# Kernel optimization log

Measured on AMD Instinct MI355X. Metric: run time of the kernel, lower is better.

The kernel has to match this reference:

```python
import jax, jax.numpy as jnp
import numpy as np

SEQ_LEN, IN_DIM = 120, 132
UNITS = (64, 128, 64)
N_LABELS = 101


def _lstm(x, W, U, b):
    """Keras-style LSTM with activation='relu', recurrent_activation='sigmoid'.
    x: (B,T,D), W: (D,4u), U: (u,4u), b: (4u,). Gate order i,f,c,o.
    Returns full hidden sequence (B,T,u)."""
    u = U.shape[0]
    # precompute input projections for all timesteps (big GEMM outside scan)
    xz = jnp.einsum('btd,dz->btz', x, W) + b  # (B,T,4u)

    def step(carry, z_t):
        h, c = carry
        z = z_t + h @ U  # (B,4u)
        i, f, g, o = jnp.split(z, 4, axis=-1)
        i = jax.nn.sigmoid(i)
        f = jax.nn.sigmoid(f)
        o = jax.nn.sigmoid(o)
        c = f * c + i * jax.nn.relu(g)
        h = o * jax.nn.relu(c)
        return (h, c), h

    B = x.shape[0]
    h0 = jnp.zeros((B, u), x.dtype)
    (_, _), hs = jax.lax.scan(step, (h0, h0), jnp.swapaxes(xz, 0, 1))
    return jnp.swapaxes(hs, 0, 1)  # (B,T,u)


def setup_inputs() -> dict:
    key = jax.random.key(0)
    ks = jax.random.split(key, 16)
    s = 0.05
    d = {'x': jax.random.normal(ks[0], (1024, SEQ_LEN, IN_DIM), jnp.float32)}
    in_dims = (IN_DIM,) + UNITS[:-1]
    for l, (din, u) in enumerate(zip(in_dims, UNITS), start=1):
        d[f'W{l}'] = jax.random.normal(ks[3 * l - 2], (din, 4 * u), jnp.float32) * s
        d[f'U{l}'] = jax.random.normal(ks[3 * l - 1], (u, 4 * u), jnp.float32) * s
        d[f'b{l}'] = jnp.zeros((4 * u,), jnp.float32)
    dense_dims = [(UNITS[-1], 64), (64, 32), (32, N_LABELS)]
    for l, (din, dout) in enumerate(dense_dims, start=1):
        d[f'Wd{l}'] = jax.random.normal(ks[9 + l], (din, dout), jnp.float32) * s
        d[f'bd{l}'] = jnp.zeros((dout,), jnp.float32)
    return d


def reference(x, W1, U1, b1, W2, U2, b2, W3, U3, b3,
              Wd1, bd1, Wd2, bd2, Wd3, bd3):
    h = _lstm(x, W1, U1, b1)          # (B,T,64)
    h = _lstm(h, W2, U2, b2)          # (B,T,128)
    h = _lstm(h, W3, U3, b3)[:, -1]   # return_sequences=False -> (B,64)
    h = jax.nn.relu(h @ Wd1 + bd1)    # (B,64)
    h = jax.nn.relu(h @ Wd2 + bd2)    # (B,32)
    return jax.nn.softmax(h @ Wd3 + bd3, axis=-1)  # (B,101)
```

## Files before the change

### kernel.cpp

```cpp
#include <hip/hip_runtime.h>
#include <math.h>

#define T_STEPS 120
#define BATCH   1024

typedef __attribute__((ext_vector_type(8))) short bf16x8;
typedef __attribute__((ext_vector_type(4))) float f32x4;
typedef unsigned short u16;

__device__ __forceinline__ unsigned split2(float f) {
    union { float f; unsigned u; } a; a.f = f;
    unsigned hi = a.u >> 16;
    union { float f; unsigned u; } h; h.u = a.u & 0xFFFF0000u;
    union { float f; unsigned u; } b; b.f = f - h.f;
    unsigned rr = b.u + 0x7FFFu + ((b.u >> 16) & 1);
    return (hi << 16) | (rr >> 16);
}

__device__ __forceinline__ short bf16rne(float f) {
    union { float f; unsigned u; } a; a.f = f;
    unsigned r = a.u + 0x7FFFu + ((a.u >> 16) & 1);
    return (short)(r >> 16);
}

__device__ __forceinline__ float fast_sigmoid(float x) {
    float e = __expf(-x);
    return __builtin_amdgcn_rcpf(1.f + e);
}

__device__ __forceinline__ void block_sync_lds() {
    asm volatile("s_waitcnt lgkmcnt(0)" ::: "memory");
    __builtin_amdgcn_sched_barrier(0);
    __builtin_amdgcn_s_barrier();
    __builtin_amdgcn_sched_barrier(0);
}

__global__ __launch_bounds__(256)
void xconv(const float* __restrict__ x, u16* __restrict__ xhi)
{
    int idx = blockIdx.x * 256 + threadIdx.x;
    int k   = idx % 144;
    int bt  = idx / 144;
    float f = (k < 132) ? x[(size_t)bt * 132 + k] : 0.f;
    xhi[idx] = (u16)(unsigned short)bf16rne(f);
}

template<int U, int KXD, int KTX, int KTAIL, int TPB, bool XLO, bool LAST_ONLY>
__global__ __launch_bounds__(TPB, 1)
void lstm_fused(const u16* __restrict__ xhi, const u16* __restrict__ xlo,
                const float* __restrict__ W, int KIN,
                const float* __restrict__ Uw, const float* __restrict__ bias,
                u16* __restrict__ hhi, u16* __restrict__ hlo,
                float* __restrict__ hlast)
{
    constexpr int NZ  = 4 * U;
    constexpr int KTH = U / 32;
    constexpr int NB  = 16;
    constexpr int HPLANE = NB * U;
    constexpr int NGRP = U / 16;
    constexpr int XPSTRIDE = 20;
    static_assert(TPB == NGRP * 128, "h-waves + x-waves");

    __shared__ u16 hsh[4 * HPLANE];
    __shared__ float xp[2 * NZ * XPSTRIDE];

    const int tid  = threadIdx.x;
    const int lane = tid & 63;
    const int wid  = tid >> 6;
    const int ln   = lane & 15;
    const int lq   = lane >> 4;
    const bool ish = (wid < NGRP);
    const int g    = ish ? wid : wid - NGRP;
    const int unit = g * 16 + ln;
    const int b0   = blockIdx.x * NB;

    if (ish) {
        bf16x8 bwu[4][KTH];
#pragma unroll
        for (int p = 0; p < 4; ++p)
#pragma unroll
            for (int kt = 0; kt < KTH; ++kt)
#pragma unroll
                for (int e = 0; e < 8; ++e) {
                    int k = kt * 32 + lq * 8 + e;
                    bwu[p][kt][e] = bf16rne(Uw[(size_t)k * NZ + p * U + unit]);
                }
        float breg[4];
#pragma unroll
        for (int p = 0; p < 4; ++p) breg[p] = bias[p * U + unit];

        u16* hw0 = hsh + ((unit >> 3) * NB + lq * 4) * 8 + (unit & 7);
        u16* hw1 = hw0 + 2 * HPLANE;
        float creg[4];
#pragma unroll
        for (int r = 0; r < 4; ++r) {
            creg[r] = 0.f;
            hw0[r * 8] = 0;
            hw0[HPLANE + r * 8] = 0;
        }

        const u16* hrd[2][KTH];
#pragma unroll
        for (int b = 0; b < 2; ++b)
#pragma unroll
            for (int kt = 0; kt < KTH; ++kt)
                hrd[b][kt] = hsh + b * 2 * HPLANE + ((kt * 4 + lq) * NB + ln) * 8;

        const float* xprd[2];
        xprd[0] = xp;
        xprd[1] = xp + (size_t)NZ * XPSTRIDE;

        size_t ho = ((size_t)(b0 + lq * 4) * T_STEPS) * U + unit;

        block_sync_lds();

#define HSTEP(CUR, OTH, tc)                                                     \
    {                                                                           \
        f32x4 acc[4];                                                           \
        _Pragma("unroll")                                                       \
        for (int p = 0; p < 4; ++p) {                                           \
            f32x4 v = *reinterpret_cast<const f32x4*>(                          \
                xprd[CUR] + (p * U + unit) * XPSTRIDE + lq * 4);                \
            acc[p][0] = v[0] + breg[p]; acc[p][1] = v[1] + breg[p];             \
            acc[p][2] = v[2] + breg[p]; acc[p][3] = v[3] + breg[p];             \
        }                                                                       \
        _Pragma("unroll")                                                       \
        for (int kt = 0; kt < KTH; ++kt) {                                      \
            bf16x8 ahh = *reinterpret_cast<const bf16x8*>(hrd[CUR][kt]);        \
            bf16x8 ahl = *reinterpret_cast<const bf16x8*>(hrd[CUR][kt] + HPLANE); \
            _Pragma("unroll")                                                   \
            for (int p = 0; p < 4; ++p) {                                       \
                acc[p] = __builtin_amdgcn_mfma_f32_16x16x32_bf16(ahh, bwu[p][kt], acc[p], 0, 0, 0); \
                acc[p] = __builtin_amdgcn_mfma_f32_16x16x32_bf16(ahl, bwu[p][kt], acc[p], 0, 0, 0); \
            }                                                                   \
        }                                                                       \
        _Pragma("unroll")                                                       \
        for (int r = 0; r < 4; ++r) {                                           \
            float si = fast_sigmoid(acc[0][r]);                                 \
            float sf = fast_sigmoid(acc[1][r]);                                 \
            float gg = fmaxf(acc[2][r], 0.f);                                   \
            float so = fast_sigmoid(acc[3][r]);                                 \
            float c  = sf * creg[r] + si * gg;                                  \
            creg[r] = c;                                                        \
            float h = so * fmaxf(c, 0.f);                                       \
            unsigned s = split2(h);                                             \
            u16* hw = (OTH) ? hw1 : hw0;                                        \
            hw[r * 8] = (u16)(s >> 16);                                         \
            hw[HPLANE + r * 8] = (u16)s;                                        \
            if constexpr (!LAST_ONLY) {                                         \
                size_t o = ho + (size_t)r * (T_STEPS * U) + (size_t)(tc) * U;   \
                hhi[o] = (u16)(s >> 16);                                        \
                hlo[o] = (u16)s;                                                \
            } else {                                                            \
                if ((tc) == T_STEPS - 1)                                        \
                    hlast[(size_t)(b0 + lq * 4 + r) * U + unit] = h;            \
            }                                                                   \
        }                                                                       \
        block_sync_lds();                                                       \
    }

        for (int t = 0; t < T_STEPS; t += 2) {
            HSTEP(0, 1, t)
            HSTEP(1, 0, t + 1)
        }
#undef HSTEP
    } else {
        bf16x8 wxw[KTX][4];
#pragma unroll
        for (int kt = 0; kt < KTX; ++kt)
#pragma unroll
            for (int p = 0; p < 4; ++p)
#pragma unroll
                for (int e = 0; e < 8; ++e) {
                    int k = kt * 32 + lq * 8 + e;
                    wxw[kt][p][e] = (k < KIN) ? bf16rne(W[(size_t)k * NZ + p * U + unit])
                                              : (short)0;
                }

        const u16* pxh = xhi + ((size_t)(b0 + ln) * T_STEPS) * KXD + lq * 8;
        const u16* pxl = XLO ? (xlo + ((size_t)(b0 + ln) * T_STEPS) * KXD + lq * 8) : nullptr;

        float* xpw[2];
        xpw[0] = xp;
        xpw[1] = xp + (size_t)NZ * XPSTRIDE;

        bf16x8 xfh[KTX] = {}, xfl[KTX] = {};
#pragma unroll
        for (int kt = 0; kt < KTX; ++kt)
            if (kt < KTX - 1 || lq < KTAIL) {
                xfh[kt] = *reinterpret_cast<const bf16x8*>(pxh + kt * 32);
                if constexpr (XLO)
                    xfl[kt] = *reinterpret_cast<const bf16x8*>(pxl + kt * 32);
            }

        {
            f32x4 xacc[4] = {};
#pragma unroll
            for (int kt = 0; kt < KTX; ++kt)
#pragma unroll
                for (int p = 0; p < 4; ++p) {
                    xacc[p] = __builtin_amdgcn_mfma_f32_16x16x32_bf16(xfh[kt], wxw[kt][p], xacc[p], 0, 0, 0);
                    if constexpr (XLO)
                        xacc[p] = __builtin_amdgcn_mfma_f32_16x16x32_bf16(xfl[kt], wxw[kt][p], xacc[p], 0, 0, 0);
                }
#pragma unroll
            for (int p = 0; p < 4; ++p)
                *reinterpret_cast<f32x4*>(xpw[0] + (p * U + unit) * XPSTRIDE + lq * 4) = xacc[p];
            pxh += KXD; if constexpr (XLO) pxl += KXD;
#pragma unroll
            for (int kt = 0; kt < KTX; ++kt)
                if (kt < KTX - 1 || lq < KTAIL) {
                    xfh[kt] = *reinterpret_cast<const bf16x8*>(pxh + kt * 32);
                    if constexpr (XLO)
                        xfl[kt] = *reinterpret_cast<const bf16x8*>(pxl + kt * 32);
                }
        }

        block_sync_lds();

#define XSTEP(OTH, tc)                                                          \
    {                                                                           \
        if ((tc) + 1 < T_STEPS) {                                               \
            f32x4 xacc[4] = {};                                                 \
            _Pragma("unroll")                                                   \
            for (int kt = 0; kt < KTX; ++kt)                                    \
            _Pragma("unroll")                                                   \
            for (int p = 0; p < 4; ++p) {                                       \
                xacc[p] = __builtin_amdgcn_mfma_f32_16x16x32_bf16(xfh[kt], wxw[kt][p], xacc[p], 0, 0, 0); \
                if constexpr (XLO)                                              \
                    xacc[p] = __builtin_amdgcn_mfma_f32_16x16x32_bf16(xfl[kt], wxw[kt][p], xacc[p], 0, 0, 0); \
            }                                                                   \
            _Pragma("unroll")                                                   \
            for (int p = 0; p < 4; ++p)                                         \
                *reinterpret_cast<f32x4*>(xpw[OTH] + (p * U + unit) * XPSTRIDE + lq * 4) = xacc[p]; \
            if ((tc) + 2 < T_STEPS) {                                           \
                pxh += KXD; if constexpr (XLO) pxl += KXD;                      \
                _Pragma("unroll")                                               \
                for (int kt = 0; kt < KTX; ++kt)                                \
                    if (kt < KTX - 1 || lq < KTAIL) {                           \
                        xfh[kt] = *reinterpret_cast<const bf16x8*>(pxh + kt * 32); \
                        if constexpr (XLO)                                      \
                            xfl[kt] = *reinterpret_cast<const bf16x8*>(pxl + kt * 32); \
                    }                                                           \
            }                                                                   \
        }                                                                       \
        block_sync_lds();                                                       \
    }

        for (int t = 0; t < T_STEPS; t += 2) {
            XSTEP(1, t)
            XSTEP(0, t + 1)
        }
#undef XSTEP
    }
}

__global__ __launch_bounds__(256)
void dense_head(const float* __restrict__ h3,
                const float* __restrict__ Wd1, const float* __restrict__ bd1,
                const float* __restrict__ Wd2, const float* __restrict__ bd2,
                const float* __restrict__ Wd3, const float* __restrict__ bd3,
                float* __restrict__ out)
{
    __shared__ float s1[4][64];
    __shared__ float s2[4][32];
    const int w    = threadIdx.x >> 6;
    const int lane = threadIdx.x & 63;
    const int row  = blockIdx.x * 4 + w;

    float hval = h3[(size_t)row * 64 + lane];
    float a = bd1[lane];
#pragma unroll
    for (int k = 0; k < 64; ++k) {
        float hk = __shfl(hval, k, 64);
        a = fmaf(hk, Wd1[k * 64 + lane], a);
    }
    s1[w][lane] = fmaxf(a, 0.f);
    __syncthreads();

    if (lane < 32) {
        float a2 = bd2[lane];
#pragma unroll
        for (int k = 0; k < 64; ++k) a2 = fmaf(s1[w][k], Wd2[k * 32 + lane], a2);
        s2[w][lane] = fmaxf(a2, 0.f);
    }
    __syncthreads();

    float a0 = bd3[lane];
#pragma unroll
    for (int k = 0; k < 32; ++k) a0 = fmaf(s2[w][k], Wd3[k * 101 + lane], a0);
    float a1 = -INFINITY;
    if (lane < 37) {
        a1 = bd3[64 + lane];
#pragma unroll
        for (int k = 0; k < 32; ++k) a1 = fmaf(s2[w][k], Wd3[k * 101 + 64 + lane], a1);
    }

    float m = fmaxf(a0, a1);
#pragma unroll
    for (int off = 32; off > 0; off >>= 1) m = fmaxf(m, __shfl_xor(m, off, 64));
    float e0 = expf(a0 - m);
    float e1 = (lane < 37) ? expf(a1 - m) : 0.f;
    float s = e0 + e1;
#pragma unroll
    for (int off = 32; off > 0; off >>= 1) s += __shfl_xor(s, off, 64);

    out[(size_t)row * 101 + lane] = e0 / s;
    if (lane < 37) out[(size_t)row * 101 + 64 + lane] = e1 / s;
}

extern "C" void kernel_launch(void* const* d_in, const int* in_sizes, int n_in,
                              void* d_out, int out_size, void* d_ws, size_t ws_size,
                              hipStream_t stream) {
    const float* x   = (const float*)d_in[0];
    const float* W1  = (const float*)d_in[1];
    const float* U1  = (const float*)d_in[2];
    const float* b1  = (const float*)d_in[3];
    const float* W2  = (const float*)d_in[4];
    const float* U2  = (const float*)d_in[5];
    const float* b2  = (const float*)d_in[6];
    const float* W3  = (const float*)d_in[7];
    const float* U3  = (const float*)d_in[8];
    const float* b3  = (const float*)d_in[9];
    const float* Wd1 = (const float*)d_in[10];
    const float* bd1 = (const float*)d_in[11];
    const float* Wd2 = (const float*)d_in[12];
    const float* bd2 = (const float*)d_in[13];
    const float* Wd3 = (const float*)d_in[14];
    const float* bd3 = (const float*)d_in[15];

    u16* ws16 = (u16*)d_ws;
    u16* xhi  = ws16;
    u16* h2hi = ws16;
    u16* h2lo = h2hi + 15728640;
    u16* h1hi = ws16 + 35389440;
    u16* h1lo = h1hi + 7864320;
    float* h3 = (float*)(ws16 + 51118080);

    xconv<<<(BATCH * T_STEPS * 144) / 256, 256, 0, stream>>>(x, xhi);
    lstm_fused<64, 144, 5, 2, 512, false, false><<<64, 512, 0, stream>>>(
        xhi, nullptr, W1, 132, U1, b1, h1hi, h1lo, nullptr);
    lstm_fused<128, 64, 2, 4, 1024, true, false><<<64, 1024, 0, stream>>>(
        h1hi, h1lo, W2, 64, U2, b2, h2hi, h2lo, nullptr);
    lstm_fused<64, 128, 4, 4, 512, true, true><<<64, 512, 0, stream>>>(
        h2hi, h2lo, W3, 128, U3, b3, nullptr, nullptr, h3);
    dense_head<<<BATCH / 4, 256, 0, stream>>>(h3, Wd1, bd1, Wd2, bd2, Wd3, bd3,
                                              (float*)d_out);
}
```

Baseline: 607.1 us.

## Fuse layer-2 input projection into recurrent waves and drop layer-1 low plane

```diff
diff --git a/kernel.cpp b/kernel.cpp
--- a/kernel.cpp
+++ b/kernel.cpp
@@ -45,8 +45,8 @@
     xhi[idx] = (u16)(unsigned short)bf16rne(f);
 }
 
-template<int U, int KXD, int KTX, int KTAIL, int TPB, bool XLO, bool LAST_ONLY>
-__global__ __launch_bounds__(TPB, 1)
+template<int U, int KXD, int KTX, int KTAIL, bool XLO, bool WLO, bool LAST_ONLY>
+__global__ __launch_bounds__(512, 1)
 void lstm_fused(const u16* __restrict__ xhi, const u16* __restrict__ xlo,
                 const float* __restrict__ W, int KIN,
                 const float* __restrict__ Uw, const float* __restrict__ bias,
@@ -59,7 +59,7 @@
     constexpr int HPLANE = NB * U;
     constexpr int NGRP = U / 16;
     constexpr int XPSTRIDE = 20;
-    static_assert(TPB == NGRP * 128, "h-waves + x-waves");
+    static_assert(NGRP * 128 == 512, "4 h-waves + 4 x-waves");
 
     __shared__ u16 hsh[4 * HPLANE];
     __shared__ float xp[2 * NZ * XPSTRIDE];
@@ -116,14 +116,12 @@
 
 #define HSTEP(CUR, OTH, tc)                                                     \
     {                                                                           \
-        f32x4 acc[4];                                                           \
-        _Pragma("unroll")                                                       \
-        for (int p = 0; p < 4; ++p) {                                           \
-            f32x4 v = *reinterpret_cast<const f32x4*>(                          \
+        f32x4 xpv[4];                                                           \
+        _Pragma("unroll")                                                       \
+        for (int p = 0; p < 4; ++p)                                             \
+            xpv[p] = *reinterpret_cast<const f32x4*>(                           \
                 xprd[CUR] + (p * U + unit) * XPSTRIDE + lq * 4);                \
-            acc[p][0] = v[0] + breg[p]; acc[p][1] = v[1] + breg[p];             \
-            acc[p][2] = v[2] + breg[p]; acc[p][3] = v[3] + breg[p];             \
-        }                                                                       \
+        f32x4 acc[4] = {};                                                      \
         _Pragma("unroll")                                                       \
         for (int kt = 0; kt < KTH; ++kt) {                                      \
             bf16x8 ahh = *reinterpret_cast<const bf16x8*>(hrd[CUR][kt]);        \
@@ -136,10 +134,14 @@
         }                                                                       \
         _Pragma("unroll")                                                       \
         for (int r = 0; r < 4; ++r) {                                           \
-            float si = fast_sigmoid(acc[0][r]);                                 \
-            float sf = fast_sigmoid(acc[1][r]);                                 \
-            float gg = fmaxf(acc[2][r], 0.f);                                   \
-            float so = fast_sigmoid(acc[3][r]);                                 \
+            float zi = acc[0][r] + xpv[0][r] + breg[0];                         \
+            float zf = acc[1][r] + xpv[1][r] + breg[1];                         \
+            float zg = acc[2][r] + xpv[2][r] + breg[2];                         \
+            float zo = acc[3][r] + xpv[3][r] + breg[3];                         \
+            float si = fast_sigmoid(zi);                                        \
+            float sf = fast_sigmoid(zf);                                        \
+            float gg = fmaxf(zg, 0.f);                                          \
+            float so = fast_sigmoid(zo);                                        \
             float c  = sf * creg[r] + si * gg;                                  \
             creg[r] = c;                                                        \
             float h = so * fmaxf(c, 0.f);                                       \
@@ -150,7 +152,7 @@
             if constexpr (!LAST_ONLY) {                                         \
                 size_t o = ho + (size_t)r * (T_STEPS * U) + (size_t)(tc) * U;   \
                 hhi[o] = (u16)(s >> 16);                                        \
-                hlo[o] = (u16)s;                                                \
+                if constexpr (WLO) hlo[o] = (u16)s;                             \
             } else {                                                            \
                 if ((tc) == T_STEPS - 1)                                        \
                     hlast[(size_t)(b0 + lq * 4 + r) * U + unit] = h;            \
@@ -253,6 +255,127 @@
         }
 #undef XSTEP
     }
+}
+
+__global__ __launch_bounds__(512, 1)
+void lstm_l2(const u16* __restrict__ xhi,
+             const float* __restrict__ W,
+             const float* __restrict__ Uw,
+             const float* __restrict__ bias,
+             u16* __restrict__ hhi, u16* __restrict__ hlo)
+{
+    constexpr int U = 128, NZ = 512, KTH = 4, NB = 16, KXD = 64, KTX = 2;
+    constexpr int HPLANE = NB * U;
+    __shared__ u16 hsh[4 * HPLANE];
+    __shared__ u16 Wl[KXD * NZ];
+
+    const int tid  = threadIdx.x;
+    const int lane = tid & 63;
+    const int wid  = tid >> 6;
+    const int ln   = lane & 15;
+    const int lq   = lane >> 4;
+    const int unit = wid * 16 + ln;
+    const int b0   = blockIdx.x * NB;
+
+    for (int idx = tid; idx < KXD * NZ; idx += 512) {
+        int k = idx >> 9, n = idx & (NZ - 1);
+        Wl[((k >> 3) * NZ + n) * 8 + (k & 7)] = (u16)bf16rne(W[(size_t)k * NZ + n]);
+    }
+
+    bf16x8 bwu[4][KTH];
+#pragma unroll
+    for (int p = 0; p < 4; ++p)
+#pragma unroll
+        for (int kt = 0; kt < KTH; ++kt)
+#pragma unroll
+            for (int e = 0; e < 8; ++e) {
+                int k = kt * 32 + lq * 8 + e;
+                bwu[p][kt][e] = bf16rne(Uw[(size_t)k * NZ + p * U + unit]);
+            }
+    float breg[4];
+#pragma unroll
+    for (int p = 0; p < 4; ++p) breg[p] = bias[p * U + unit];
+
+    u16* hw0 = hsh + ((unit >> 3) * NB + lq * 4) * 8 + (unit & 7);
+    u16* hw1 = hw0 + 2 * HPLANE;
+    float creg[4];
+#pragma unroll
+    for (int r = 0; r < 4; ++r) {
+        creg[r] = 0.f;
+        hw0[r * 8] = 0;
+        hw0[HPLANE + r * 8] = 0;
+    }
+
+    const u16* hrd[2][KTH];
+#pragma unroll
+    for (int b = 0; b < 2; ++b)
+#pragma unroll
+        for (int kt = 0; kt < KTH; ++kt)
+            hrd[b][kt] = hsh + b * 2 * HPLANE + ((kt * 4 + lq) * NB + ln) * 8;
+
+    const u16* wb = Wl + ((size_t)lq * NZ + unit) * 8;
+
+    const u16* pxh = xhi + ((size_t)(b0 + ln) * T_STEPS) * KXD + lq * 8;
+    bf16x8 xfh[KTX];
+#pragma unroll
+    for (int kt = 0; kt < KTX; ++kt)
+        xfh[kt] = *reinterpret_cast<const bf16x8*>(pxh + kt * 32);
+
+    size_t ho = ((size_t)(b0 + lq * 4) * T_STEPS) * U + unit;
+
+    block_sync_lds();
+
+#define L2STEP(CUR, OTH, tc)                                                    \
+    {                                                                           \
+        f32x4 acc[4] = {};                                                      \
+        _Pragma("unroll")                                                       \
+        for (int kt = 0; kt < KTH; ++kt) {                                      \
+            bf16x8 ahh = *reinterpret_cast<const bf16x8*>(hrd[CUR][kt]);        \
+            bf16x8 ahl = *reinterpret_cast<const bf16x8*>(hrd[CUR][kt] + HPLANE); \
+            _Pragma("unroll")                                                   \
+            for (int p = 0; p < 4; ++p) {                                       \
+                acc[p] = __builtin_amdgcn_mfma_f32_16x16x32_bf16(ahh, bwu[p][kt], acc[p], 0, 0, 0); \
+                acc[p] = __builtin_amdgcn_mfma_f32_16x16x32_bf16(ahl, bwu[p][kt], acc[p], 0, 0, 0); \
+            }                                                                   \
+        }                                                                       \
+        _Pragma("unroll")                                                       \
+        for (int kt = 0; kt < KTX; ++kt)                                        \
+        _Pragma("unroll")                                                       \
+        for (int p = 0; p < 4; ++p) {                                           \
+            bf16x8 wf = *reinterpret_cast<const bf16x8*>(wb + (kt * 4 * NZ + p * U) * 8); \
+            acc[p] = __builtin_amdgcn_mfma_f32_16x16x32_bf16(xfh[kt], wf, acc[p], 0, 0, 0); \
+        }                                                                       \
+        if ((tc) + 1 < T_STEPS) {                                               \
+            pxh += KXD;                                                         \
+            _Pragma("unroll")                                                   \
+            for (int kt = 0; kt < KTX; ++kt)                                    \
+                xfh[kt] = *reinterpret_cast<const bf16x8*>(pxh + kt * 32);      \
+        }                                                                       \
+        _Pragma("unroll")                                                       \
+        for (int r = 0; r < 4; ++r) {                                           \
+            float si = fast_sigmoid(acc[0][r] + breg[0]);                       \
+            float sf = fast_sigmoid(acc[1][r] + breg[1]);                       \
+            float gg = fmaxf(acc[2][r] + breg[2], 0.f);                         \
+            float so = fast_sigmoid(acc[3][r] + breg[3]);                       \
+            float c  = sf * creg[r] + si * gg;                                  \
+            creg[r] = c;                                                        \
+            float h = so * fmaxf(c, 0.f);                                       \
+            unsigned s = split2(h);                                             \
+            u16* hw = (OTH) ? hw1 : hw0;                                        \
+            hw[r * 8] = (u16)(s >> 16);                                         \
+            hw[HPLANE + r * 8] = (u16)s;                                        \
+            size_t o = ho + (size_t)r * (T_STEPS * U) + (size_t)(tc) * U;       \
+            hhi[o] = (u16)(s >> 16);                                            \
+            hlo[o] = (u16)s;                                                    \
+        }                                                                       \
+        block_sync_lds();                                                       \
+    }
+
+    for (int t = 0; t < T_STEPS; t += 2) {
+        L2STEP(0, 1, t)
+        L2STEP(1, 0, t + 1)
+    }
+#undef L2STEP
 }
 
 __global__ __launch_bounds__(256)
@@ -334,15 +457,13 @@
     u16* h2hi = ws16;
     u16* h2lo = h2hi + 15728640;
     u16* h1hi = ws16 + 35389440;
-    u16* h1lo = h1hi + 7864320;
     float* h3 = (float*)(ws16 + 51118080);
 
     xconv<<<(BATCH * T_STEPS * 144) / 256, 256, 0, stream>>>(x, xhi);
-    lstm_fused<64, 144, 5, 2, 512, false, false><<<64, 512, 0, stream>>>(
-        xhi, nullptr, W1, 132, U1, b1, h1hi, h1lo, nullptr);
-    lstm_fused<128, 64, 2, 4, 1024, true, false><<<64, 1024, 0, stream>>>(
-        h1hi, h1lo, W2, 64, U2, b2, h2hi, h2lo, nullptr);
-    lstm_fused<64, 128, 4, 4, 512, true, true><<<64, 512, 0, stream>>>(
+    lstm_fused<64, 144, 5, 2, false, false, false><<<64, 512, 0, stream>>>(
+        xhi, nullptr, W1, 132, U1, b1, h1hi, nullptr, nullptr);
+    lstm_l2<<<64, 512, 0, stream>>>(h1hi, W2, U2, b2, h2hi, h2lo);
+    lstm_fused<64, 128, 4, 4, true, true, true><<<64, 512, 0, stream>>>(
         h2hi, h2lo, W3, 128, U3, b3, nullptr, nullptr, h3);
     dense_head<<<BATCH / 4, 256, 0, stream>>>(h3, Wd1, bd1, Wd2, bd2, Wd3, bd3,
                                               (float*)d_out);
```

Measured after the change: 507.6 us. 16.4% less time.
